# Kernel tuning notes

Measured on AMD Instinct MI355X. Metric: run time of the kernel, lower is better.

The kernel has to match this reference:

```python
import jax, jax.numpy as jnp
import numpy as np

K = 1024          # num_embeddings
D = 256           # embedding_dim
COMMIT = 0.1      # commitment_cost
EPS = float(np.finfo(np.float32).eps)


def setup_inputs() -> dict:
    key = jax.random.key(0)
    k1, k2 = jax.random.split(key)
    X = jax.random.normal(k1, (16, 4096, D), dtype=jnp.float32)
    # matches nn.Embedding init: uniform(-1/K, 1/K)
    emb_weight = jax.random.uniform(k2, (K, D), dtype=jnp.float32,
                                    minval=-1.0 / K, maxval=1.0 / K)
    return {"X": X, "emb_weight": emb_weight}


def reference(X, emb_weight):
    B, N, Dm = X.shape
    Xf = X.reshape(-1, Dm)                                  # [BN, D]
    dist = (jnp.sum(Xf * Xf, axis=-1, keepdims=True)
            + jnp.sum(emb_weight * emb_weight, axis=-1)
            - 2.0 * Xf @ emb_weight.T)                      # [BN, K]
    idx = jnp.argmin(dist, axis=-1)                         # [BN]
    # one-hot @ codebook == gather
    quantized = emb_weight[idx].reshape(X.shape)            # [B, N, D]
    # perplexity from one-hot mean == normalized counts
    counts = jnp.zeros((K,), dtype=X.dtype).at[idx].add(1.0)
    avg_probs = counts / Xf.shape[0]
    perplexity = jnp.exp(-jnp.sum(avg_probs * jnp.log(avg_probs + EPS)))
    # vq loss (learnable codebook branch)
    sg = jax.lax.stop_gradient
    e_latent = jnp.mean((sg(quantized) - X) ** 2)
    q_latent = jnp.mean((quantized - sg(X)) ** 2)
    loss_vq = q_latent + COMMIT * e_latent
    # straight-through estimator
    quantized_st = X + sg(quantized - X)
    encoding_indices = idx.reshape(B, N)
    return quantized_st, encoding_indices, perplexity, loss_vq
```

## Files before the change

kernel.cpp:

```cpp
#include <hip/hip_runtime.h>
#include <math.h>

#define ROWS 65536
#define DIM  256
#define KC   1024
#define NQ   (ROWS * DIM)

typedef float f2 __attribute__((ext_vector_type(2)));
typedef float f4v __attribute__((ext_vector_type(4)));


__device__ __forceinline__ float half_sq_sum(const float* __restrict__ a) {
    float4 u0 = *(const float4*)(a);
    float4 u1 = *(const float4*)(a + 4);
    float r0 = __fmul_rn(u0.x, u0.x);
    float r1 = __fmul_rn(u0.y, u0.y);
    float r2 = __fmul_rn(u0.z, u0.z);
    float r3 = __fmul_rn(u0.w, u0.w);
    float r4 = __fmul_rn(u1.x, u1.x);
    float r5 = __fmul_rn(u1.y, u1.y);
    float r6 = __fmul_rn(u1.z, u1.z);
    float r7 = __fmul_rn(u1.w, u1.w);
    for (int i = 8; i < 128; i += 8) {
        float4 v0 = *(const float4*)(a + i);
        float4 v1 = *(const float4*)(a + i + 4);
        r0 = __fadd_rn(r0, __fmul_rn(v0.x, v0.x));
        r1 = __fadd_rn(r1, __fmul_rn(v0.y, v0.y));
        r2 = __fadd_rn(r2, __fmul_rn(v0.z, v0.z));
        r3 = __fadd_rn(r3, __fmul_rn(v0.w, v0.w));
        r4 = __fadd_rn(r4, __fmul_rn(v1.x, v1.x));
        r5 = __fadd_rn(r5, __fmul_rn(v1.y, v1.y));
        r6 = __fadd_rn(r6, __fmul_rn(v1.z, v1.z));
        r7 = __fadd_rn(r7, __fmul_rn(v1.w, v1.w));
    }
    float s01 = __fadd_rn(r0, r1);
    float s23 = __fadd_rn(r2, r3);
    float s45 = __fadd_rn(r4, r5);
    float s67 = __fadd_rn(r6, r7);
    return __fadd_rn(__fadd_rn(s01, s23), __fadd_rn(s45, s67));
}

__device__ __forceinline__ float sq_sum_numpy(const float* __restrict__ p) {
    float h0 = half_sq_sum(p);
    float h1 = half_sq_sum(p + 128);
    return __fadd_rn(h0, h1);
}

__global__ __launch_bounds__(256) void k_prepB(const float* __restrict__ E,
                                               float* __restrict__ B32) {
    int j = blockIdx.x * 256 + threadIdx.x;
    if (j >= KC) return;
    B32[j] = sq_sum_numpy(E + (size_t)j * DIM);
}

#define TM 128
#define TN 128
#define TD 32
#define BUFF 4096
#define BSTR 8192

#define PKL(d_, x_, e_)                                                         \
    asm("v_pk_fma_f32 %0, %1, %2, %0 op_sel:[0,0,0] op_sel_hi:[0,1,1]"          \
        : "+v"(d_) : "v"(x_), "v"(e_));
#define PKH(d_, x_, e_)                                                         \
    asm("v_pk_fma_f32 %0, %1, %2, %0 op_sel:[1,0,0] op_sel_hi:[1,1,1]"          \
        : "+v"(d_) : "v"(x_), "v"(e_));

__global__ __launch_bounds__(256, 2) void k_pass1(
    const float* __restrict__ X, const float* __restrict__ E,
    const float* __restrict__ B32, float* __restrict__ out0,
    float* __restrict__ out1, int* __restrict__ counts,
    double* __restrict__ lossacc)
{
    __shared__ __align__(16) float sm[2 * BSTR];

    const int tid = threadIdx.x;
    const int tx  = tid & 15;
    const int ty  = tid >> 4;
    const int rowbase = blockIdx.x * TM;

    float4 xv0, xv1, xv2, xv3, ev0, ev1, ev2, ev3;

#define LOADR(cbn, dcn)                                                         \
    do {                                                                        \
        int fi_, r_, d4_;                                                       \
        fi_ = tid;       r_ = fi_ >> 3; d4_ = (fi_ & 7) << 2;                   \
        xv0 = *(const float4*)(X + (size_t)(rowbase + r_) * DIM + (dcn) + d4_); \
        ev0 = *(const float4*)(E + (size_t)((cbn) + r_) * DIM + (dcn) + d4_);   \
        fi_ = tid + 256; r_ = fi_ >> 3; d4_ = (fi_ & 7) << 2;                   \
        xv1 = *(const float4*)(X + (size_t)(rowbase + r_) * DIM + (dcn) + d4_); \
        ev1 = *(const float4*)(E + (size_t)((cbn) + r_) * DIM + (dcn) + d4_);   \
        fi_ = tid + 512; r_ = fi_ >> 3; d4_ = (fi_ & 7) << 2;                   \
        xv2 = *(const float4*)(X + (size_t)(rowbase + r_) * DIM + (dcn) + d4_); \
        ev2 = *(const float4*)(E + (size_t)((cbn) + r_) * DIM + (dcn) + d4_);   \
        fi_ = tid + 768; r_ = fi_ >> 3; d4_ = (fi_ & 7) << 2;                   \
        xv3 = *(const float4*)(X + (size_t)(rowbase + r_) * DIM + (dcn) + d4_); \
        ev3 = *(const float4*)(E + (size_t)((cbn) + r_) * DIM + (dcn) + d4_);   \
    } while (0)

#define WRITE1(Xs_, Es_, v_, e_, fif_)                                          \
    do {                                                                        \
        int r_ = (fif_) >> 3, d4_ = ((fif_) & 7) << 2;                          \
        int off_ = d4_ * 128 + ((((r_) >> 2) ^ (d4_ >> 2)) << 2) + ((r_) & 3);  \
        (Xs_)[off_]       = v_.x; (Xs_)[off_ + 128] = v_.y;                     \
        (Xs_)[off_ + 256] = v_.z; (Xs_)[off_ + 384] = v_.w;                     \
        (Es_)[off_]       = e_.x; (Es_)[off_ + 128] = e_.y;                     \
        (Es_)[off_ + 256] = e_.z; (Es_)[off_ + 384] = e_.w;                     \
    } while (0)

#define WRITEB(b)                                                               \
    do {                                                                        \
        float* Xs_ = sm + (b) * BSTR;                                           \
        float* Es_ = Xs_ + BUFF;                                                \
        WRITE1(Xs_, Es_, xv0, ev0, tid);                                        \
        WRITE1(Xs_, Es_, xv1, ev1, tid + 256);                                  \
        WRITE1(Xs_, Es_, xv2, ev2, tid + 512);                                  \
        WRITE1(Xs_, Es_, xv3, ev3, tid + 768);                                  \
    } while (0)

    LOADR(0, 0);

    {
        int r = tid >> 1, h = tid & 1;
        sm[(r << 1) + h] = half_sq_sum(X + (size_t)(rowbase + r) * DIM + (h << 7));
    }
    __syncthreads();
    float a8[8];
#pragma unroll
    for (int i = 0; i < 8; ++i)
        a8[i] = __fadd_rn(sm[(ty * 8 + i) * 2], sm[(ty * 8 + i) * 2 + 1]);
    __syncthreads();
    WRITEB(0);

    float v1[8]; int i1[8];
#pragma unroll
    for (int i = 0; i < 8; ++i) { v1[i] = 3.0e38f; i1[i] = 0; }

    int cur = 0;
    for (int cb8 = 0; cb8 < 8; ++cb8) {
        const int cbase = cb8 * TN;

        f2 acc[8][4];
#pragma unroll
        for (int i = 0; i < 8; ++i)
#pragma unroll
            for (int j = 0; j < 4; ++j) acc[i][j] = (f2){0.0f, 0.0f};

        for (int dc8 = 0; dc8 < 8; ++dc8) {
            const int s = cb8 * 8 + dc8;
            __syncthreads();
            if (s < 63) {
                const int sn = s + 1;
                LOADR((sn >> 3) * TN, (sn & 7) * TD);
            }
            {
                const float* Xc = sm + cur * BSTR;
                const float* Ec = Xc + BUFF;
#pragma unroll 2
                for (int dq = 0; dq < 8; ++dq) {
                    const float* xp0 = Xc + dq * 512 + ((((ty << 1)    ) ^ dq) << 2);
                    const float* xp1 = Xc + dq * 512 + ((((ty << 1) | 1) ^ dq) << 2);
                    const float* ep0 = Ec + dq * 512 + ((tx ^ dq) << 2);
#pragma unroll
                    for (int ddi = 0; ddi < 4; ++ddi) {
                        f4v t0 = *(const f4v*)(xp0 + ddi * 128);
                        f4v t1 = *(const f4v*)(xp1 + ddi * 128);
                        f4v u0 = *(const f4v*)(ep0 + ddi * 128);
                        f4v u1 = *(const f4v*)(ep0 + ddi * 128 + 64);
                        f2 x01 = __builtin_shufflevector(t0, t0, 0, 1);
                        f2 x23 = __builtin_shufflevector(t0, t0, 2, 3);
                        f2 x45 = __builtin_shufflevector(t1, t1, 0, 1);
                        f2 x67 = __builtin_shufflevector(t1, t1, 2, 3);
                        f2 e0  = __builtin_shufflevector(u0, u0, 0, 1);
                        f2 e1  = __builtin_shufflevector(u0, u0, 2, 3);
                        f2 e2  = __builtin_shufflevector(u1, u1, 0, 1);
                        f2 e3  = __builtin_shufflevector(u1, u1, 2, 3);
                        PKL(acc[0][0], x01, e0) PKL(acc[0][1], x01, e1)
                        PKL(acc[0][2], x01, e2) PKL(acc[0][3], x01, e3)
                        PKH(acc[1][0], x01, e0) PKH(acc[1][1], x01, e1)
                        PKH(acc[1][2], x01, e2) PKH(acc[1][3], x01, e3)
                        PKL(acc[2][0], x23, e0) PKL(acc[2][1], x23, e1)
                        PKL(acc[2][2], x23, e2) PKL(acc[2][3], x23, e3)
                        PKH(acc[3][0], x23, e0) PKH(acc[3][1], x23, e1)
                        PKH(acc[3][2], x23, e2) PKH(acc[3][3], x23, e3)
                        PKL(acc[4][0], x45, e0) PKL(acc[4][1], x45, e1)
                        PKL(acc[4][2], x45, e2) PKL(acc[4][3], x45, e3)
                        PKH(acc[5][0], x45, e0) PKH(acc[5][1], x45, e1)
                        PKH(acc[5][2], x45, e2) PKH(acc[5][3], x45, e3)
                        PKL(acc[6][0], x67, e0) PKL(acc[6][1], x67, e1)
                        PKL(acc[6][2], x67, e2) PKL(acc[6][3], x67, e3)
                        PKH(acc[7][0], x67, e0) PKH(acc[7][1], x67, e1)
                        PKH(acc[7][2], x67, e2) PKH(acc[7][3], x67, e3)
                    }
                }
            }
            if (s < 63) WRITEB(cur ^ 1);
            cur ^= 1;
        }

        float4 bq0 = *(const float4*)(B32 + cbase + (tx << 2));
        float4 bq1 = *(const float4*)(B32 + cbase + 64 + (tx << 2));
        float bvv[8] = {bq0.x, bq0.y, bq0.z, bq0.w, bq1.x, bq1.y, bq1.z, bq1.w};
#pragma unroll
        for (int j = 0; j < 8; ++j) {
            const int c = cbase + ((j < 4) ? ((tx << 2) + j)
                                           : (64 + (tx << 2) + (j - 4)));
#pragma unroll
            for (int i = 0; i < 8; ++i) {
                float av  = acc[i][j >> 1][j & 1];
                float Cv  = __fmul_rn(2.0f, av);
                float t1v = __fadd_rn(a8[i], bvv[j]);
                float dv  = __fsub_rn(t1v, Cv);
                if (dv < v1[i]) { v1[i] = dv; i1[i] = c; }
            }
        }
    }

    __syncthreads();
    float* Mv   = sm;
    int*   Mi   = (int*)(sm + 2048);
    int*   sIdx = (int*)(sm + 4096);
    double* wsum = (double*)(sm + 4224);
#pragma unroll
    for (int i = 0; i < 8; ++i) {
        int r = ty * 8 + i;
        Mv[r * 16 + tx] = v1[i];
        Mi[r * 16 + tx] = i1[i];
    }
    __syncthreads();
    if (tid < TM) {
        int r = tid;
        float bv = Mv[r * 16];
        int   bi = Mi[r * 16];
        for (int t = 1; t < 16; ++t) {
            float av = Mv[r * 16 + t];
            int   ai = Mi[r * 16 + t];
            if (av < bv || (av == bv && ai < bi)) { bv = av; bi = ai; }
        }
        sIdx[r] = bi;
        out1[rowbase + r] = (float)bi;
        atomicAdd(&counts[bi], 1);
    }
    __syncthreads();

    const size_t base = (size_t)rowbase * DIM;
    double s = 0.0;
#pragma unroll 4
    for (int g = 0; g < 32; ++g) {
        int fi  = tid + g * 256;
        int row = fi >> 6;
        int d4  = fi & 63;
        int j = sIdx[row];
        float4 q = *(const float4*)(E + (size_t)j * DIM + d4 * 4);
        float4 x = *(const float4*)(X + base + (size_t)fi * 4);
        *(float4*)(out0 + base + (size_t)fi * 4) = q;
        double dx;
        dx = (double)q.x - (double)x.x; s = fma(dx, dx, s);
        dx = (double)q.y - (double)x.y; s = fma(dx, dx, s);
        dx = (double)q.z - (double)x.z; s = fma(dx, dx, s);
        dx = (double)q.w - (double)x.w; s = fma(dx, dx, s);
    }
#pragma unroll
    for (int off = 32; off > 0; off >>= 1) s += __shfl_down(s, off, 64);
    int lane = tid & 63, wv = tid >> 6;
    if (lane == 0) wsum[wv] = s;
    __syncthreads();
    if (tid == 0) {
        double t = wsum[0] + wsum[1] + wsum[2] + wsum[3];
        atomicAdd(lossacc, t);
    }
#undef LOADR
#undef WRITE1
#undef WRITEB
}

__global__ void k_fin(const int* __restrict__ counts,
                      const double* __restrict__ lossacc,
                      float* __restrict__ out_pl)
{
    __shared__ double sh[256];
    double s = 0.0;
    for (int i = threadIdx.x; i < KC; i += 256) {
        double p = (double)counts[i] / 65536.0;
        s += p * log(p + 1.1920928955078125e-07);
    }
    sh[threadIdx.x] = s;
    __syncthreads();
    for (int off = 128; off > 0; off >>= 1) {
        if (threadIdx.x < off) sh[threadIdx.x] += sh[threadIdx.x + off];
        __syncthreads();
    }
    if (threadIdx.x == 0) {
        out_pl[0] = (float)exp(-sh[0]);
        out_pl[1] = (float)((*lossacc / (double)NQ) * 1.1);
    }
}

extern "C" void kernel_launch(void* const* d_in, const int* in_sizes, int n_in,
                              void* d_out, int out_size, void* d_ws, size_t ws_size,
                              hipStream_t stream) {
    const float* X = (const float*)d_in[0];
    const float* E = (const float*)d_in[1];
    float* out = (float*)d_out;
    char* ws = (char*)d_ws;

    double* lossacc = (double*)(ws + 0);
    int*    counts  = (int*)(ws + 16);
    float*  B32     = (float*)(ws + 4224);

    hipMemsetAsync(d_ws, 0, 4224, stream);

    hipLaunchKernelGGL(k_prepB, dim3(4),         dim3(256), 0, stream, E, B32);
    hipLaunchKernelGGL(k_pass1, dim3(ROWS / TM), dim3(256), 0, stream,
                       X, E, B32, out, out + NQ, counts, lossacc);
    hipLaunchKernelGGL(k_fin,   dim3(1),         dim3(256), 0, stream,
                       counts, lossacc, out + NQ + 65536);
}
```

Baseline: 518.0 us.

## Use split-bf16 MFMA distance GEMM with near-tie fp32 recheck

Replaces the fp32 packed-FMA distance GEMM with bf16 MFMA using a hi/lo split (three products) to approximate fp32 accuracy. Rows whose best and second-best distances lie within a threshold are flagged and recomputed exactly in fp32 by a separate kernel. The output gather, loss and histogram move into their own kernels. This removes the FMA-bound fp32 matmul cost but adds conversion passes over X and E, scratch traffic through the output buffer, and more launches. Correctness of the argmin depends on the threshold covering the bf16 split error.

After: 833.6 us. 1.61x slower.

```diff
diff --git a/kernel.cpp b/kernel.cpp
--- a/kernel.cpp
+++ b/kernel.cpp
@@ -8,7 +8,12 @@
 
 typedef float f2 __attribute__((ext_vector_type(2)));
 typedef float f4v __attribute__((ext_vector_type(4)));
-
+typedef short bf16x8 __attribute__((ext_vector_type(8)));
+typedef float f32x4  __attribute__((ext_vector_type(4)));
+
+#define WS_REQ 1851392
+
+#define THRESH 4.0e-4f
 
 __device__ __forceinline__ float half_sq_sum(const float* __restrict__ a) {
     float4 u0 = *(const float4*)(a);
@@ -46,6 +51,340 @@
     return __fadd_rn(h0, h1);
 }
 
+__device__ __forceinline__ ushort bf16_rne(float f) {
+    unsigned u = __float_as_uint(f);
+    unsigned r = u + 0x7FFFu + ((u >> 16) & 1u);
+    return (ushort)(r >> 16);
+}
+__device__ __forceinline__ float bf16_tof(ushort h) {
+    return __uint_as_float(((unsigned)h) << 16);
+}
+
+
+__global__ __launch_bounds__(256) void k_prepE(const float* __restrict__ E,
+                                               float* __restrict__ B32,
+                                               ushort* __restrict__ Ehi,
+                                               ushort* __restrict__ Elo) {
+    int j = blockIdx.x * 256 + threadIdx.x;
+    if (j >= KC) return;
+    const float* p = E + (size_t)j * DIM;
+    B32[j] = sq_sum_numpy(p);
+    for (int d4 = 0; d4 < DIM; d4 += 4) {
+        float4 v = *(const float4*)(p + d4);
+        ushort h0 = bf16_rne(v.x), h1 = bf16_rne(v.y);
+        ushort h2 = bf16_rne(v.z), h3 = bf16_rne(v.w);
+        ushort l0 = bf16_rne(v.x - bf16_tof(h0));
+        ushort l1 = bf16_rne(v.y - bf16_tof(h1));
+        ushort l2 = bf16_rne(v.z - bf16_tof(h2));
+        ushort l3 = bf16_rne(v.w - bf16_tof(h3));
+        uint2 ph, pl;
+        ph.x = (unsigned)h0 | ((unsigned)h1 << 16);
+        ph.y = (unsigned)h2 | ((unsigned)h3 << 16);
+        pl.x = (unsigned)l0 | ((unsigned)l1 << 16);
+        pl.y = (unsigned)l2 | ((unsigned)l3 << 16);
+        *(uint2*)(Ehi + (size_t)j * DIM + d4) = ph;
+        *(uint2*)(Elo + (size_t)j * DIM + d4) = pl;
+    }
+}
+
+__global__ __launch_bounds__(256) void k_prepX(const float* __restrict__ X,
+                                               ushort* __restrict__ Xhi,
+                                               ushort* __restrict__ Xlo) {
+    size_t g = (size_t)(blockIdx.x * 256 + threadIdx.x) * 8;
+    float4 a = *(const float4*)(X + g);
+    float4 b = *(const float4*)(X + g + 4);
+    float f[8] = {a.x, a.y, a.z, a.w, b.x, b.y, b.z, b.w};
+    ushort h[8], l[8];
+#pragma unroll
+    for (int i = 0; i < 8; ++i) {
+        h[i] = bf16_rne(f[i]);
+        l[i] = bf16_rne(f[i] - bf16_tof(h[i]));
+    }
+    uint4 ph, pl;
+    ph.x = (unsigned)h[0] | ((unsigned)h[1] << 16);
+    ph.y = (unsigned)h[2] | ((unsigned)h[3] << 16);
+    ph.z = (unsigned)h[4] | ((unsigned)h[5] << 16);
+    ph.w = (unsigned)h[6] | ((unsigned)h[7] << 16);
+    pl.x = (unsigned)l[0] | ((unsigned)l[1] << 16);
+    pl.y = (unsigned)l[2] | ((unsigned)l[3] << 16);
+    pl.z = (unsigned)l[4] | ((unsigned)l[5] << 16);
+    pl.w = (unsigned)l[6] | ((unsigned)l[7] << 16);
+    *(uint4*)(Xhi + g) = ph;
+    *(uint4*)(Xlo + g) = pl;
+}
+
+#define TBYTE(r_, q_) ((r_) * 64 + ((((q_) + ((r_) >> 1)) & 3) << 4))
+
+__global__ __launch_bounds__(256) void k_pass1f(
+    const float* __restrict__ X,
+    const ushort* __restrict__ Xhi_g, const ushort* __restrict__ Xlo_g,
+    const ushort* __restrict__ Ehi_g, const ushort* __restrict__ Elo_g,
+    const float* __restrict__ B32g, float* __restrict__ Arr,
+    int* __restrict__ idx32, int* __restrict__ flagcnt,
+    int* __restrict__ flaglist)
+{
+    __shared__ __align__(16) char smB[65536];
+    float* smf = (float*)smB;
+
+    const int tid = threadIdx.x;
+    const int w   = tid >> 6;
+    const int lane = tid & 63;
+    const int q4  = lane >> 4;
+    const int l15 = lane & 15;
+    const int rowbase = blockIdx.x * 128;
+    const int ra0 = w * 32 + l15;
+    const int ra1 = ra0 + 16;
+
+    uint4 stg[8];
+
+#define FLOAD(cbn, chn)                                                         \
+    do {                                                                        \
+        _Pragma("unroll")                                                       \
+        for (int i_ = 0; i_ < 8; ++i_) {                                        \
+            int g_ = tid + ((i_ & 1) << 8);                                     \
+            int r_ = g_ >> 2, qq_ = g_ & 3;                                     \
+            size_t off_ = (size_t)(chn) * 32 + qq_ * 8;                         \
+            const ushort* src_;                                                 \
+            if ((i_ >> 1) == 0)                                                 \
+                src_ = Xhi_g + (size_t)(rowbase + r_) * DIM + off_;             \
+            else if ((i_ >> 1) == 1)                                            \
+                src_ = Xlo_g + (size_t)(rowbase + r_) * DIM + off_;             \
+            else if ((i_ >> 1) == 2)                                            \
+                src_ = Ehi_g + (size_t)((cbn) + r_) * DIM + off_;               \
+            else                                                                \
+                src_ = Elo_g + (size_t)((cbn) + r_) * DIM + off_;               \
+            stg[i_] = *(const uint4*)src_;                                      \
+        }                                                                       \
+    } while (0)
+
+#define FWRITE(b)                                                               \
+    do {                                                                        \
+        char* base_ = smB + (b) * 32768;                                        \
+        _Pragma("unroll")                                                       \
+        for (int i_ = 0; i_ < 8; ++i_) {                                        \
+            int g_ = tid + ((i_ & 1) << 8);                                     \
+            int r_ = g_ >> 2, qq_ = g_ & 3;                                     \
+            *(uint4*)(base_ + (i_ >> 1) * 8192 + TBYTE(r_, qq_)) = stg[i_];     \
+        }                                                                       \
+    } while (0)
+
+    FLOAD(0, 0);
+
+    {
+        int r = tid >> 1, h = tid & 1;
+        smf[(r << 1) + h] = half_sq_sum(X + (size_t)(rowbase + r) * DIM + (h << 7));
+    }
+    __syncthreads();
+    float a8[8];
+#pragma unroll
+    for (int s = 0; s < 8; ++s) {
+        int row = w * 32 + (s >> 2) * 16 + q4 * 4 + (s & 3);
+        a8[s] = __fadd_rn(smf[row * 2], smf[row * 2 + 1]);
+    }
+    if (tid < 128)
+        Arr[rowbase + tid] = __fadd_rn(smf[tid * 2], smf[tid * 2 + 1]);
+    __syncthreads();
+    FWRITE(0);
+
+    float v1[8], v2[8]; int i1[8];
+#pragma unroll
+    for (int s = 0; s < 8; ++s) { v1[s] = 3.0e38f; v2[s] = 3.0e38f; i1[s] = 0; }
+
+    int cur = 0;
+    for (int cb = 0; cb < 8; ++cb) {
+        f32x4 acc0[8], acc1[8];
+#pragma unroll
+        for (int cf = 0; cf < 8; ++cf) {
+            acc0[cf] = (f32x4){0.f, 0.f, 0.f, 0.f};
+            acc1[cf] = (f32x4){0.f, 0.f, 0.f, 0.f};
+        }
+        for (int ch = 0; ch < 8; ++ch) {
+            const int s = cb * 8 + ch;
+            __syncthreads();
+            if (s < 63) { const int sn = s + 1; FLOAD((sn >> 3) * 128, (sn & 7)); }
+            {
+                const char* Xh = smB + cur * 32768;
+                const char* Xl = Xh + 8192;
+                const char* Eh = Xh + 16384;
+                const char* El = Xh + 24576;
+                bf16x8 ah0 = *(const bf16x8*)(Xh + TBYTE(ra0, q4));
+                bf16x8 ah1 = *(const bf16x8*)(Xh + TBYTE(ra1, q4));
+                bf16x8 al0 = *(const bf16x8*)(Xl + TBYTE(ra0, q4));
+                bf16x8 al1 = *(const bf16x8*)(Xl + TBYTE(ra1, q4));
+#pragma unroll
+                for (int cf = 0; cf < 8; ++cf) {
+                    int rc = cf * 16 + l15;
+                    bf16x8 bh = *(const bf16x8*)(Eh + TBYTE(rc, q4));
+                    bf16x8 bl = *(const bf16x8*)(El + TBYTE(rc, q4));
+                    acc0[cf] = __builtin_amdgcn_mfma_f32_16x16x32_bf16(ah0, bh, acc0[cf], 0, 0, 0);
+                    acc0[cf] = __builtin_amdgcn_mfma_f32_16x16x32_bf16(ah0, bl, acc0[cf], 0, 0, 0);
+                    acc0[cf] = __builtin_amdgcn_mfma_f32_16x16x32_bf16(al0, bh, acc0[cf], 0, 0, 0);
+                    acc1[cf] = __builtin_amdgcn_mfma_f32_16x16x32_bf16(ah1, bh, acc1[cf], 0, 0, 0);
+                    acc1[cf] = __builtin_amdgcn_mfma_f32_16x16x32_bf16(ah1, bl, acc1[cf], 0, 0, 0);
+                    acc1[cf] = __builtin_amdgcn_mfma_f32_16x16x32_bf16(al1, bh, acc1[cf], 0, 0, 0);
+                }
+            }
+            if (s < 63) FWRITE(cur ^ 1);
+            cur ^= 1;
+        }
+#pragma unroll
+        for (int cf = 0; cf < 8; ++cf) {
+            const int c = cb * 128 + cf * 16 + l15;
+            const float b = B32g[c];
+#pragma unroll
+            for (int reg = 0; reg < 4; ++reg) {
+                {
+                    float dv = __fsub_rn(__fadd_rn(a8[reg], b),
+                                         __fmul_rn(2.0f, acc0[cf][reg]));
+                    if (dv < v1[reg]) { v2[reg] = v1[reg]; v1[reg] = dv; i1[reg] = c; }
+                    else if (dv < v2[reg]) v2[reg] = dv;
+                }
+                {
+                    float dv = __fsub_rn(__fadd_rn(a8[4 + reg], b),
+                                         __fmul_rn(2.0f, acc1[cf][reg]));
+                    if (dv < v1[4 + reg]) { v2[4 + reg] = v1[4 + reg]; v1[4 + reg] = dv; i1[4 + reg] = c; }
+                    else if (dv < v2[4 + reg]) v2[4 + reg] = dv;
+                }
+            }
+        }
+    }
+
+    __syncthreads();
+    float* Mv = (float*)smB;
+    int*   Mi = (int*)(smB + 8192);
+    float* M2 = (float*)(smB + 16384);
+#pragma unroll
+    for (int s = 0; s < 8; ++s) {
+        int row = w * 32 + (s >> 2) * 16 + q4 * 4 + (s & 3);
+        Mv[row * 16 + l15] = v1[s];
+        Mi[row * 16 + l15] = i1[s];
+        M2[row * 16 + l15] = v2[s];
+    }
+    __syncthreads();
+    if (tid < 128) {
+        float bv1 = Mv[tid * 16]; int bi = Mi[tid * 16]; float bv2 = M2[tid * 16];
+        for (int t = 1; t < 16; ++t) {
+            float av1 = Mv[tid * 16 + t];
+            int   ai  = Mi[tid * 16 + t];
+            float av2 = M2[tid * 16 + t];
+            if (av1 < bv1) { bv2 = fminf(bv1, av2); bv1 = av1; bi = ai; }
+            else           { bv2 = fminf(bv2, av1); }
+        }
+        idx32[rowbase + tid] = bi;
+        if (bv2 - bv1 <= THRESH) {
+            int slot = atomicAdd(flagcnt, 1);
+            flaglist[slot] = rowbase + tid;
+        }
+    }
+#undef FLOAD
+#undef FWRITE
+}
+
+__global__ __launch_bounds__(256) void k_recheck(
+    const float* __restrict__ X, const float* __restrict__ E,
+    const float* __restrict__ B32, const float* __restrict__ Arr,
+    const int* __restrict__ flaglist, const int* __restrict__ flagcnt,
+    int* __restrict__ idx32)
+{
+    __shared__ float xr[256];
+    __shared__ float Et[256 * 33];
+    __shared__ float rv[256];
+    __shared__ int   rc[256];
+    const int tid = threadIdx.x;
+    const int nf = *flagcnt;
+    for (int f = blockIdx.x; f < nf; f += gridDim.x) {
+        const int row = flaglist[f];
+        __syncthreads();
+        xr[tid] = X[(size_t)row * DIM + tid];
+        const float A = Arr[row];
+        float bestv = 3.0e38f; int bestc = 0;
+        for (int cp = 0; cp < 4; ++cp) {
+            float acc = 0.0f;
+            for (int dch = 0; dch < 8; ++dch) {
+                __syncthreads();
+#pragma unroll
+                for (int i = 0; i < 8; ++i) {
+                    int g = tid + i * 256;
+                    int r = g >> 3, d4 = (g & 7) * 4;
+                    float4 v = *(const float4*)(E + (size_t)(cp * 256 + r) * DIM
+                                                + dch * 32 + d4);
+                    Et[r * 33 + d4 + 0] = v.x; Et[r * 33 + d4 + 1] = v.y;
+                    Et[r * 33 + d4 + 2] = v.z; Et[r * 33 + d4 + 3] = v.w;
+                }
+                __syncthreads();
+#pragma unroll
+                for (int dd = 0; dd < 32; ++dd)
+                    acc = fmaf(xr[dch * 32 + dd], Et[tid * 33 + dd], acc);
+            }
+            const int c = cp * 256 + tid;
+            float dv = __fsub_rn(__fadd_rn(A, B32[c]), __fmul_rn(2.0f, acc));
+            if (dv < bestv) { bestv = dv; bestc = c; }
+        }
+        rv[tid] = bestv; rc[tid] = bestc;
+        __syncthreads();
+        for (int off = 128; off > 0; off >>= 1) {
+            if (tid < off) {
+                float av = rv[tid + off]; int ac = rc[tid + off];
+                if (av < rv[tid] || (av == rv[tid] && ac < rc[tid])) {
+                    rv[tid] = av; rc[tid] = ac;
+                }
+            }
+            __syncthreads();
+        }
+        if (tid == 0) idx32[row] = rc[0];
+    }
+}
+
+__global__ __launch_bounds__(256) void k_out(
+    const float* __restrict__ X, const float* __restrict__ E,
+    const int* __restrict__ idx32, float* __restrict__ out0,
+    double* __restrict__ lossacc)
+{
+    const int NF4 = NQ / 4;
+    double s = 0.0;
+    for (int g = blockIdx.x * blockDim.x + threadIdx.x; g < NF4;
+         g += gridDim.x * blockDim.x) {
+        int row = g >> 6;
+        int d4  = g & 63;
+        int j = idx32[row];
+        float4 q = *(const float4*)(E + (size_t)j * DIM + d4 * 4);
+        float4 x = *(const float4*)(X + (size_t)g * 4);
+        *(float4*)(out0 + (size_t)g * 4) = q;
+        double dx;
+        dx = (double)q.x - (double)x.x; s = fma(dx, dx, s);
+        dx = (double)q.y - (double)x.y; s = fma(dx, dx, s);
+        dx = (double)q.z - (double)x.z; s = fma(dx, dx, s);
+        dx = (double)q.w - (double)x.w; s = fma(dx, dx, s);
+    }
+#pragma unroll
+    for (int off = 32; off > 0; off >>= 1) s += __shfl_down(s, off, 64);
+    __shared__ double wsum[4];
+    int lane = threadIdx.x & 63, wv = threadIdx.x >> 6;
+    if (lane == 0) wsum[wv] = s;
+    __syncthreads();
+    if (threadIdx.x == 0) {
+        double t = wsum[0] + wsum[1] + wsum[2] + wsum[3];
+        atomicAdd(lossacc, t);
+    }
+}
+
+__global__ __launch_bounds__(256) void k_idxout(
+    const int* __restrict__ idx32, float* __restrict__ out1,
+    int* __restrict__ counts)
+{
+    __shared__ int h[KC];
+    for (int i = threadIdx.x; i < KC; i += 256) h[i] = 0;
+    __syncthreads();
+    int r = blockIdx.x * 256 + threadIdx.x;
+    int j = idx32[r];
+    out1[r] = (float)j;
+    atomicAdd(&h[j], 1);
+    __syncthreads();
+    for (int i = threadIdx.x; i < KC; i += 256)
+        if (h[i]) atomicAdd(&counts[i], h[i]);
+}
+
+
 __global__ __launch_bounds__(256) void k_prepB(const float* __restrict__ E,
                                                float* __restrict__ B32) {
     int j = blockIdx.x * 256 + threadIdx.x;
@@ -66,7 +405,7 @@
     asm("v_pk_fma_f32 %0, %1, %2, %0 op_sel:[1,0,0] op_sel_hi:[1,1,1]"          \
         : "+v"(d_) : "v"(x_), "v"(e_));
 
-__global__ __launch_bounds__(256, 2) void k_pass1(
+__global__ __launch_bounds__(256, 2) void k_pass1_fb(
     const float* __restrict__ X, const float* __restrict__ E,
     const float* __restrict__ B32, float* __restrict__ out0,
     float* __restrict__ out1, int* __restrict__ counts,
@@ -119,7 +458,6 @@
     } while (0)
 
     LOADR(0, 0);
-
     {
         int r = tid >> 1, h = tid & 1;
         sm[(r << 1) + h] = half_sq_sum(X + (size_t)(rowbase + r) * DIM + (h << 7));
@@ -139,7 +477,6 @@
     int cur = 0;
     for (int cb8 = 0; cb8 < 8; ++cb8) {
         const int cbase = cb8 * TN;
-
         f2 acc[8][4];
 #pragma unroll
         for (int i = 0; i < 8; ++i)
@@ -308,11 +645,35 @@
     int*    counts  = (int*)(ws + 16);
     float*  B32     = (float*)(ws + 4224);
 
-    hipMemsetAsync(d_ws, 0, 4224, stream);
-
-    hipLaunchKernelGGL(k_prepB, dim3(4),         dim3(256), 0, stream, E, B32);
-    hipLaunchKernelGGL(k_pass1, dim3(ROWS / TM), dim3(256), 0, stream,
-                       X, E, B32, out, out + NQ, counts, lossacc);
-    hipLaunchKernelGGL(k_fin,   dim3(1),         dim3(256), 0, stream,
-                       counts, lossacc, out + NQ + 65536);
-}
+    if (ws_size >= (size_t)WS_REQ) {
+        int*    flagcnt  = (int*)(ws + 8320);
+        int*    flaglist = (int*)(ws + 16384);
+        int*    idx32    = (int*)(ws + 278528);
+        float*  Arr      = (float*)(ws + 540672);
+        ushort* Ehi      = (ushort*)(ws + 802816);
+        ushort* Elo      = (ushort*)(ws + 1327104);
+        ushort* Xhi      = (ushort*)out;
+        ushort* Xlo      = Xhi + (size_t)NQ;
+
+        hipMemsetAsync(d_ws, 0, 8336, stream);
+        hipLaunchKernelGGL(k_prepE, dim3(4),    dim3(256), 0, stream, E, B32, Ehi, Elo);
+        hipLaunchKernelGGL(k_prepX, dim3(8192), dim3(256), 0, stream, X, Xhi, Xlo);
+        hipLaunchKernelGGL(k_pass1f, dim3(512), dim3(256), 0, stream,
+                           X, Xhi, Xlo, Ehi, Elo, B32, Arr, idx32, flagcnt, flaglist);
+        hipLaunchKernelGGL(k_recheck, dim3(2048), dim3(256), 0, stream,
+                           X, E, B32, Arr, flaglist, flagcnt, idx32);
+        hipLaunchKernelGGL(k_out,    dim3(2048), dim3(256), 0, stream,
+                           X, E, idx32, out, lossacc);
+        hipLaunchKernelGGL(k_idxout, dim3(256),  dim3(256), 0, stream,
+                           idx32, out + NQ, counts);
+        hipLaunchKernelGGL(k_fin,    dim3(1),    dim3(256), 0, stream,
+                           counts, lossacc, out + NQ + 65536);
+    } else {
+        hipMemsetAsync(d_ws, 0, 4224, stream);
+        hipLaunchKernelGGL(k_prepB, dim3(4),          dim3(256), 0, stream, E, B32);
+        hipLaunchKernelGGL(k_pass1_fb, dim3(ROWS / TM), dim3(256), 0, stream,
+                           X, E, B32, out, out + NQ, counts, lossacc);
+        hipLaunchKernelGGL(k_fin,   dim3(1),          dim3(256), 0, stream,
+                           counts, lossacc, out + NQ + 65536);
+    }
+}
```
